# Optimization experiments

Measured on AMD Instinct MI355X. Metric: run time of the kernel, lower is better.

## Reference

```python
import jax, jax.numpy as jnp
import numpy as np
import math

MAX_SIZE = 2048  # max_size init arg


def setup_inputs() -> dict:
    key = jax.random.key(0)
    k1, k2, k3 = jax.random.split(key, 3)
    B, S, D = 16, 1024, 512
    PRED = 256
    data = jax.random.normal(k1, (B, S, D), dtype=jnp.float32)
    W = jax.random.normal(k2, (PRED, D), dtype=jnp.float32) * (1.0 / math.sqrt(D))
    b = jax.random.normal(k3, (PRED,), dtype=jnp.float32) * 0.01
    return {"data": data, "W": W, "b": b}


def reference(data, W, b):
    # data: [B, S, D]; self-attention with q=k=v=data
    B, S, D = data.shape
    pred_len = W.shape[0]
    scale = 1.0 / math.sqrt(D)
    scores = jnp.einsum('bsd,btd->bst', data, data) * scale          # [B,S,S]
    prob = jax.nn.softmax(scores, axis=-1)
    attn = jnp.einsum('bst,btd->bsd', prob, data)                     # [B,S,D]
    # NOTE: the original concatenates a 'mask' block (rows S..2S) onto attn,
    # but the per-timestep Linear loop only reads rows 0..S-1, so the mask
    # never affects the output (dead code). The loop collapses to one GEMM.
    lin = jnp.einsum('bsd,pd->bsp', attn, W) + b                      # [B,S,pred_len]
    out = jnp.zeros((B, MAX_SIZE, pred_len), dtype=data.dtype)
    out = out.at[:, :S, :].set(lin)
    return out
```

## Files before the change

### kernel.cpp

```cpp
#include <hip/hip_runtime.h>
#include <cstdint>
#include <cstddef>

#define B_    16
#define S_    1024
#define D_    512
#define P_    256
#define MAXS_ 2048

typedef unsigned short u16;
typedef unsigned int   u32;
typedef _Float16 f16;
typedef _Float16 f16x8 __attribute__((ext_vector_type(8)));
typedef float  f32x4  __attribute__((ext_vector_type(4)));
typedef unsigned short u16x4 __attribute__((ext_vector_type(4)));
typedef unsigned short u16x8 __attribute__((ext_vector_type(8)));

__device__ __forceinline__ void gld_lds16(const void* g, void* l) {
  __builtin_amdgcn_global_load_lds(
      (const __attribute__((address_space(1))) u32*)g,
      (__attribute__((address_space(3))) u32*)l, 16, 0, 0);
}

__device__ __forceinline__ u16 f2h(float f) {
  return __builtin_bit_cast(u16, (f16)f);
}
__device__ __forceinline__ float h2f(u16 h) {
  return (float)__builtin_bit_cast(f16, h);
}

template<int BPB>
__device__ __forceinline__ void xcd_map(int L, int& bz, int& r) {
  const int t = L & 7;
  const int j = L >> 3;
  bz = (t << 1) | (j / BPB);
  r  = j % BPB;
}

__global__ void convert_f16_kernel(const float* __restrict__ src, u16* __restrict__ dst, long n4) {
  long stride = (long)gridDim.x * blockDim.x;
  for (long i = (long)blockIdx.x * blockDim.x + threadIdx.x; i < n4; i += stride) {
    float4 v = ((const float4*)src)[i];
    u16x4 o;
    o[0] = f2h(v.x); o[1] = f2h(v.y); o[2] = f2h(v.z); o[3] = f2h(v.w);
    ((u16x4*)dst)[i] = o;
  }
}

__global__ __launch_bounds__(512, 2) void qk_pipe(
    const u16* __restrict__ A, u16* __restrict__ Cout,
    float2* __restrict__ rowpart, float scale) {
  extern __shared__ __align__(16) char smem[];
  const int tid  = threadIdx.x;
  const int lane = tid & 63;
  const int w    = tid >> 6;
  const int wm   = w >> 2;
  const int wn   = w & 3;
  const int lr   = lane & 15;
  const int hi   = lane >> 4;

  const int L = blockIdx.x + (blockIdx.y << 2) + (blockIdx.z << 4);
  int bz, r;
  xcd_map<16>(L, bz, r);
  const int I0 = (r >> 2) * 256;
  const int J0 = (r & 3) * 256;
  const u16* Ab = A + (long)bz * (S_ * D_);

  auto stageP = [&](int s, int part) {
    if (s >= 16) return;
    char* dst = smem + (s & 3) * 32768 + part * 16384;
    const int base = part ? J0 : I0;
    const int k0 = s * 32;
    #pragma unroll
    for (int i = 0; i < 2; ++i) {
      int cid   = i * 512 + tid;
      int inner = cid >> 2;
      int c     = (cid & 3) ^ ((inner >> 1) & 3);
      gld_lds16(Ab + (size_t)(base + inner) * D_ + k0 + c * 8, dst + cid * 16);
    }
  };

  f32x4 acc[8][4] = {};

  stageP(0, 0); stageP(0, 1);
  stageP(1, 0); stageP(1, 1);
  stageP(2, 0); stageP(2, 1);
  asm volatile("s_waitcnt vmcnt(8)" ::: "memory");
  __builtin_amdgcn_s_barrier();

  for (int s = 0; s < 16; ++s) {
    const char* sl = smem + (s & 3) * 32768;
    f16x8 af0[4], af1[4], bf[4];
    #pragma unroll
    for (int mq = 0; mq < 4; ++mq) {
      int row = wm * 128 + mq * 16 + lr;
      int cp  = hi ^ ((row >> 1) & 3);
      af0[mq] = *(const f16x8*)(sl + row * 64 + cp * 16);
    }
    #pragma unroll
    for (int mq = 0; mq < 4; ++mq) {
      int row = wm * 128 + 64 + mq * 16 + lr;
      int cp  = hi ^ ((row >> 1) & 3);
      af1[mq] = *(const f16x8*)(sl + row * 64 + cp * 16);
    }
    #pragma unroll
    for (int n = 0; n < 4; ++n) {
      int row = wn * 64 + n * 16 + lr;
      int cp  = hi ^ ((row >> 1) & 3);
      bf[n] = *(const f16x8*)(sl + 16384 + row * 64 + cp * 16);
    }
    stageP(s + 3, 0);
    stageP(s + 3, 1);
    asm volatile("s_waitcnt lgkmcnt(0)" ::: "memory");
    __builtin_amdgcn_sched_barrier(0);
    __builtin_amdgcn_s_setprio(1);
    #pragma unroll
    for (int mq = 0; mq < 4; ++mq)
      #pragma unroll
      for (int n = 0; n < 4; ++n)
        acc[mq][n] = __builtin_amdgcn_mfma_f32_16x16x32_f16(af0[mq], bf[n], acc[mq][n], 0, 0, 0);
    #pragma unroll
    for (int mq = 0; mq < 4; ++mq)
      #pragma unroll
      for (int n = 0; n < 4; ++n)
        acc[4 + mq][n] = __builtin_amdgcn_mfma_f32_16x16x32_f16(af1[mq], bf[n], acc[4 + mq][n], 0, 0, 0);
    __builtin_amdgcn_s_setprio(0);
    if (s <= 12)      asm volatile("s_waitcnt vmcnt(8)" ::: "memory");
    else if (s == 13) asm volatile("s_waitcnt vmcnt(4)" ::: "memory");
    else if (s == 14) asm volatile("s_waitcnt vmcnt(0)" ::: "memory");
    __builtin_amdgcn_s_barrier();
  }

  __syncthreads();
  float2* part = (float2*)smem;
  const float l2e = 1.4426950408889634f;
  u16* Cb = Cout + (long)bz * S_ * S_;
  const int row0 = I0 + wm * 128;
  const int col0 = J0 + wn * 64;
  #pragma unroll
  for (int m = 0; m < 8; ++m) {
    #pragma unroll
    for (int i = 0; i < 4; ++i) {
      int rr = row0 + m * 16 + (hi << 2) + i;
      float v[4];
      #pragma unroll
      for (int n = 0; n < 4; ++n) v[n] = acc[m][n][i] * scale;
      float mx = fmaxf(fmaxf(v[0], v[1]), fmaxf(v[2], v[3]));
      #pragma unroll
      for (int off = 1; off <= 8; off <<= 1)
        mx = fmaxf(mx, __shfl_xor(mx, off));
      float sum = 0.f;
      #pragma unroll
      for (int n = 0; n < 4; ++n) sum += exp2f((v[n] - mx) * l2e);
      #pragma unroll
      for (int off = 1; off <= 8; off <<= 1)
        sum += __shfl_xor(sum, off);
      #pragma unroll
      for (int n = 0; n < 4; ++n)
        Cb[(size_t)rr * S_ + col0 + n * 16 + lr] = f2h(v[n]);
      if (lr == 0)
        part[(wm * 128 + m * 16 + (hi << 2) + i) * 4 + wn] = make_float2(mx, sum);
    }
  }
  __syncthreads();
  if (tid < 256) {
    float2 a = part[tid * 4],     b = part[tid * 4 + 1];
    float2 c = part[tid * 4 + 2], d = part[tid * 4 + 3];
    float m = fmaxf(fmaxf(a.x, b.x), fmaxf(c.x, d.x));
    float l = a.y * exp2f((a.x - m) * l2e) + b.y * exp2f((b.x - m) * l2e)
            + c.y * exp2f((c.x - m) * l2e) + d.y * exp2f((d.x - m) * l2e);
    rowpart[((long)bz * 4 + (J0 >> 8)) * S_ + I0 + tid] = make_float2(m, l);
  }
}

__global__ __launch_bounds__(256, 2) void pv_slot(
    const u16* __restrict__ scores, const u16* __restrict__ VWT,
    const float2* __restrict__ rowpart,
    float* __restrict__ out, const float* __restrict__ bias) {
  extern __shared__ __align__(16) char smem[];
  const int tid  = threadIdx.x;
  const int lane = tid & 63;
  const int w    = tid >> 6;
  const int wm   = w >> 1;
  const int wn   = w & 1;
  const int lr   = lane & 15;
  const int hi   = lane >> 4;

  const int L = blockIdx.x + (blockIdx.y << 1) + (blockIdx.z << 6);
  int bz, rblk;
  xcd_map<64>(L, bz, rblk);
  const int yt = rblk >> 1;
  const int J0 = (rblk & 1) * 128;

  float* ob = out + (long)bz * MAXS_ * P_;
  if (yt >= 16) {
    #pragma unroll 2
    for (int i = tid; i < 64 * 32; i += 256) {
      int rr = i >> 5;
      int c4 = i & 31;
      *((float4*)(ob + (size_t)(yt * 64 + rr) * P_ + J0) + c4) =
          make_float4(0.f, 0.f, 0.f, 0.f);
    }
    return;
  }

  const int q0 = yt * 64;
  const u16* sA = scores + ((long)bz * S_ + q0) * S_;
  const u16* Vb = VWT + (long)bz * P_ * S_ + (size_t)J0 * S_;
  const float l2e = 1.4426950408889634f;

  const int ar0 = tid >> 3;
  const int ar1 = 32 + (tid >> 3);
  const int ac  = tid & 7;
  const int c0  = ac ^ (ar0 & 7);
  const int c1  = ac ^ (ar1 & 7);

  const float2* rp = rowpart + (long)bz * 4 * S_;
  auto mergeStat = [&](int row, float& nml, float& il) {
    float2 a = rp[row],          b = rp[S_ + row];
    float2 c = rp[2 * S_ + row], d = rp[3 * S_ + row];
    float m = fmaxf(fmaxf(a.x, b.x), fmaxf(c.x, d.x));
    float l = a.y * exp2f((a.x - m) * l2e) + b.y * exp2f((b.x - m) * l2e)
            + c.y * exp2f((c.x - m) * l2e) + d.y * exp2f((d.x - m) * l2e);
    nml = -m * l2e;
    il  = 1.f / l;
  };
  float nml0, il0, nml1, il1;
  mergeStat(q0 + ar0, nml0, il0);
  mergeStat(q0 + ar1, nml1, il1);

  auto loadA = [&](int s, u16x8 (&r)[2]) {
    r[0] = *(const u16x8*)(sA + (size_t)ar0 * S_ + s * 64 + c0 * 8);
    r[1] = *(const u16x8*)(sA + (size_t)ar1 * S_ + s * 64 + c1 * 8);
  };
  auto writeA = [&](int buf, u16x8 (&r)[2]) {
    char* dA = smem + buf * 8192;
    u16x8 p0, p1;
    #pragma unroll
    for (int j = 0; j < 8; ++j) {
      p0[j] = f2h(exp2f(fmaf(h2f(r[0][j]), l2e, nml0)) * il0);
      p1[j] = f2h(exp2f(fmaf(h2f(r[1][j]), l2e, nml1)) * il1);
    }
    *(u16x8*)(dA + (size_t)tid * 16)         = p0;
    *(u16x8*)(dA + (size_t)(256 + tid) * 16) = p1;
  };
  auto stageB = [&](int s, int buf) {
    char* dB = smem + 24576 + buf * 16384;
    #pragma unroll
    for (int i = 0; i < 4; ++i) {
      int cid = i * 256 + tid;
      int row = cid >> 3;
      int c   = (cid & 7) ^ (row & 7);
      gld_lds16(Vb + (size_t)row * S_ + s * 64 + c * 8, dB + cid * 16);
    }
  };

  f32x4 acc[2][4] = {};
  u16x8 rA[2][2];

  loadA(0, rA[0]);
  __builtin_amdgcn_sched_barrier(0);
  stageB(0, 0);
  __builtin_amdgcn_sched_barrier(0);
  loadA(1, rA[1]);
  __builtin_amdgcn_sched_barrier(0);
  stageB(1, 1);
  __builtin_amdgcn_sched_barrier(0);
  asm volatile("s_waitcnt vmcnt(6)" ::: "memory");
  writeA(0, rA[0]);
  asm volatile("s_waitcnt lgkmcnt(0)" ::: "memory");
  __builtin_amdgcn_s_barrier();

  #pragma unroll
  for (int s = 0; s < 16; ++s) {
    const int bufR = s % 3;
    const char* aB = smem + bufR * 8192;
    const char* bB = smem + 24576 + bufR * 16384;

    f16x8 af[2][2], bf[2][4];
    #pragma unroll
    for (int kk = 0; kk < 2; ++kk) {
      #pragma unroll
      for (int m = 0; m < 2; ++m) {
        int row = wm * 32 + m * 16 + lr;
        int cp  = (kk * 4 + hi) ^ (row & 7);
        af[kk][m] = *(const f16x8*)(aB + row * 128 + cp * 16);
      }
      #pragma unroll
      for (int n = 0; n < 4; ++n) {
        int row = wn * 64 + n * 16 + lr;
        int cp  = (kk * 4 + hi) ^ (row & 7);
        bf[kk][n] = *(const f16x8*)(bB + row * 128 + cp * 16);
      }
    }

    if (s + 2 < 16) {
      loadA(s + 2, rA[s & 1]);
      __builtin_amdgcn_sched_barrier(0);
      stageB(s + 2, (s + 2) % 3);
      __builtin_amdgcn_sched_barrier(0);
    }

    __builtin_amdgcn_s_setprio(1);
    #pragma unroll
    for (int kk = 0; kk < 2; ++kk)
      #pragma unroll
      for (int m = 0; m < 2; ++m)
        #pragma unroll
        for (int n = 0; n < 4; ++n)
          acc[m][n] = __builtin_amdgcn_mfma_f32_16x16x32_f16(
              af[kk][m], bf[kk][n], acc[m][n], 0, 0, 0);
    __builtin_amdgcn_s_setprio(0);

    if (s < 15) {
      if (s <= 13) asm volatile("s_waitcnt vmcnt(6)" ::: "memory");
      else         asm volatile("s_waitcnt vmcnt(0)" ::: "memory");
      writeA((s + 1) % 3, rA[(s + 1) & 1]);
      asm volatile("s_waitcnt lgkmcnt(0)" ::: "memory");
      __builtin_amdgcn_s_barrier();
    }
  }

  float bv[4];
  #pragma unroll
  for (int n = 0; n < 4; ++n) bv[n] = bias[J0 + wn * 64 + n * 16 + lr];
  #pragma unroll
  for (int m = 0; m < 2; ++m) {
    #pragma unroll
    for (int i = 0; i < 4; ++i) {
      int rr = q0 + wm * 32 + m * 16 + (hi << 2) + i;
      #pragma unroll
      for (int n = 0; n < 4; ++n)
        ob[(size_t)rr * P_ + J0 + wn * 64 + n * 16 + lr] = acc[m][n][i] + bv[n];
    }
  }
}

template<int KK, int BM, int BN, int NW, int WNS, int BPB>
__global__ __launch_bounds__(NW * 64, 2) void gemm_nt_small(
    const u16* __restrict__ A, const u16* __restrict__ Bm,
    u16* __restrict__ C, long sAb, long sBb, long sCb, int LDC) {
  constexpr int T   = NW * 64;
  constexpr int WMS = NW / WNS;
  constexpr int MF  = BM / (WMS * 16);
  constexpr int NF  = BN / (WNS * 16);
  constexpr int LA  = BM * 8 / T;
  constexpr int LB  = BN * 8 / T;
  constexpr int SZ  = (BM + BN) * 128;
  constexpr int NT  = KK / 64;

  extern __shared__ __align__(16) char smem[];
  const int tid  = threadIdx.x;
  const int lane = tid & 63;
  const int w    = tid >> 6;
  const int wm   = w / WNS;
  const int wn   = w % WNS;
  const int lr   = lane & 15;
  const int hi   = lane >> 4;

  const int L = blockIdx.x + gridDim.x * (blockIdx.y + gridDim.y * blockIdx.z);
  int bz, r;
  xcd_map<BPB>(L, bz, r);
  const int I0 = (r / gridDim.x) * BM;
  const int J0 = (r % gridDim.x) * BN;
  const u16* Ab = A  + (long)bz * sAb;
  const u16* Bb = Bm + (long)bz * sBb;

  auto stage = [&](int buf, int k0) {
    char* sA = smem + buf * SZ;
    char* sB = sA + BM * 128;
    #pragma unroll
    for (int i = 0; i < LA; ++i) {
      int cid = i * T + tid;
      int row = cid >> 3;
      int c   = (cid & 7) ^ (row & 7);
      gld_lds16(Ab + (size_t)(I0 + row) * KK + k0 + c * 8, sA + cid * 16);
    }
    #pragma unroll
    for (int i = 0; i < LB; ++i) {
      int cid = i * T + tid;
      int row = cid >> 3;
      int c   = (cid & 7) ^ (row & 7);
      gld_lds16(Bb + (size_t)(J0 + row) * KK + k0 + c * 8, sB + cid * 16);
    }
  };

  f32x4 acc[MF][NF] = {};
  stage(0, 0);
  for (int t = 0; t < NT; ++t) {
    const char* lA = smem + (t & 1) * SZ;
    const char* lB = lA + BM * 128;
    if (t + 1 < NT) {
      stage((t + 1) & 1, (t + 1) * 64);
      asm volatile("s_waitcnt vmcnt(%0)" :: "i"(LA + LB) : "memory");
    } else {
      asm volatile("s_waitcnt vmcnt(0)" ::: "memory");
    }
    __builtin_amdgcn_s_barrier();
    __builtin_amdgcn_sched_barrier(0);
    #pragma unroll
    for (int kk = 0; kk < 2; ++kk) {
      f16x8 af[MF], bfv[NF];
      #pragma unroll
      for (int m = 0; m < MF; ++m) {
        int row = wm * (MF * 16) + m * 16 + lr;
        int cp  = (kk * 4 + hi) ^ (row & 7);
        af[m] = *(const f16x8*)(lA + ((row * 8 + cp) << 4));
      }
      #pragma unroll
      for (int n = 0; n < NF; ++n) {
        int row = wn * (NF * 16) + n * 16 + lr;
        int cp  = (kk * 4 + hi) ^ (row & 7);
        bfv[n] = *(const f16x8*)(lB + ((row * 8 + cp) << 4));
      }
      __builtin_amdgcn_s_setprio(1);
      #pragma unroll
      for (int m = 0; m < MF; ++m)
        #pragma unroll
        for (int n = 0; n < NF; ++n)
          acc[m][n] = __builtin_amdgcn_mfma_f32_16x16x32_f16(af[m], bfv[n], acc[m][n], 0, 0, 0);
      __builtin_amdgcn_s_setprio(0);
    }
    __builtin_amdgcn_sched_barrier(0);
    __builtin_amdgcn_s_barrier();
  }

  const int row0 = I0 + wm * (MF * 16);
  const int col0 = J0 + wn * (NF * 16);
  #pragma unroll
  for (int m = 0; m < MF; ++m)
    #pragma unroll
    for (int i = 0; i < 4; ++i) {
      int rr = row0 + m * 16 + (hi << 2) + i;
      #pragma unroll
      for (int n = 0; n < NF; ++n)
        C[(long)bz * sCb + (size_t)rr * LDC + col0 + n * 16 + lr] = f2h(acc[m][n][i]);
    }
}

extern "C" void kernel_launch(void* const* d_in, const int* in_sizes, int n_in,
                              void* d_out, int out_size, void* d_ws, size_t ws_size,
                              hipStream_t stream) {
  const float* data = (const float*)d_in[0];
  const float* W    = (const float*)d_in[1];
  const float* bias = (const float*)d_in[2];
  float* out = (float*)d_out;
  char*  ws  = (char*)d_ws;

  const size_t MB = 1024 * 1024;
  u16*    dataH   = (u16*)(ws);
  u16*    Wh      = (u16*)(ws + 16 * MB);
  u16*    scoresH = (u16*)(ws + 17 * MB);
  u16*    VWT     = (u16*)(ws + 49 * MB);
  float2* rowpart = (float2*)(ws + 57 * MB);

  const float scale = 0.04419417382415922f;

  constexpr int SMEM_QK = 4 * 32768;
  constexpr int SMEM_PV = 3 * 8192 + 3 * 16384;
  constexpr int SMEM_VW = 2 * (64 + 128) * 128;

  (void)hipFuncSetAttribute((const void*)&qk_pipe,
                      hipFuncAttributeMaxDynamicSharedMemorySize, SMEM_QK);
  (void)hipFuncSetAttribute((const void*)&pv_slot,
                      hipFuncAttributeMaxDynamicSharedMemorySize, SMEM_PV);
  (void)hipFuncSetAttribute((const void*)&gemm_nt_small<512, 64, 128, 4, 2, 32>,
                      hipFuncAttributeMaxDynamicSharedMemorySize, SMEM_VW);

  convert_f16_kernel<<<2048, 256, 0, stream>>>(data, dataH, (long)B_ * S_ * D_ / 4);
  convert_f16_kernel<<<64, 256, 0, stream>>>(W, Wh, (long)P_ * D_ / 4);

  gemm_nt_small<512, 64, 128, 4, 2, 32><<<dim3(8, 4, 16), 256, SMEM_VW, stream>>>(
      Wh, dataH, VWT, 0L, (long)S_ * D_, (long)P_ * S_, S_);

  qk_pipe<<<dim3(4, 4, 16), 512, SMEM_QK, stream>>>(
      dataH, scoresH, rowpart, scale);

  pv_slot<<<dim3(2, 32, 16), 256, SMEM_PV, stream>>>(
      scoresH, VWT, rowpart, out, bias);
}
```

Before: 78.39 us.

## Shrink QK tile to 128x128 with 4 waves and 3-stage pipeline

The QK^T kernel moves from 256x256 tiles with 8 waves and a 4-deep LDS ring to 128x128 tiles with 4 waves and a 3-deep ring. This quadruples the grid to 1024 blocks for better CU fill and occupancy. The per-row softmax partials are now split into 8 column slices, so the PV kernel merges 8 partial max/sum pairs per row instead of 4. The smaller tiles lower arithmetic intensity and raise global and L2 traffic for the QK operands.

After: 80.42 us. +2.6%, slower.

```diff
diff --git a/kernel.cpp b/kernel.cpp
--- a/kernel.cpp
+++ b/kernel.cpp
@@ -47,86 +47,77 @@
   }
 }
 
-__global__ __launch_bounds__(512, 2) void qk_pipe(
+__global__ __launch_bounds__(256, 3) void qk_pipe(
     const u16* __restrict__ A, u16* __restrict__ Cout,
     float2* __restrict__ rowpart, float scale) {
   extern __shared__ __align__(16) char smem[];
   const int tid  = threadIdx.x;
   const int lane = tid & 63;
   const int w    = tid >> 6;
-  const int wm   = w >> 2;
-  const int wn   = w & 3;
+  const int wm   = w >> 1;
+  const int wn   = w & 1;
   const int lr   = lane & 15;
   const int hi   = lane >> 4;
 
-  const int L = blockIdx.x + (blockIdx.y << 2) + (blockIdx.z << 4);
+  const int L = blockIdx.x + (blockIdx.y << 3) + (blockIdx.z << 6);
   int bz, r;
-  xcd_map<16>(L, bz, r);
-  const int I0 = (r >> 2) * 256;
-  const int J0 = (r & 3) * 256;
+  xcd_map<64>(L, bz, r);
+  const int I0 = (r >> 3) * 128;
+  const int J0 = (r & 7) * 128;
   const u16* Ab = A + (long)bz * (S_ * D_);
 
-  auto stageP = [&](int s, int part) {
+  auto stage = [&](int s) {
     if (s >= 16) return;
-    char* dst = smem + (s & 3) * 32768 + part * 16384;
-    const int base = part ? J0 : I0;
+    char* dst = smem + (s % 3) * 16384;
     const int k0 = s * 32;
     #pragma unroll
     for (int i = 0; i < 2; ++i) {
-      int cid   = i * 512 + tid;
-      int inner = cid >> 2;
-      int c     = (cid & 3) ^ ((inner >> 1) & 3);
-      gld_lds16(Ab + (size_t)(base + inner) * D_ + k0 + c * 8, dst + cid * 16);
-    }
-  };
-
-  f32x4 acc[8][4] = {};
-
-  stageP(0, 0); stageP(0, 1);
-  stageP(1, 0); stageP(1, 1);
-  stageP(2, 0); stageP(2, 1);
-  asm volatile("s_waitcnt vmcnt(8)" ::: "memory");
+      int cid = i * 256 + tid;
+      int row = cid >> 2;
+      int c   = (cid & 3) ^ ((row >> 1) & 3);
+      gld_lds16(Ab + (size_t)(I0 + row) * D_ + k0 + c * 8, dst + cid * 16);
+    }
+    #pragma unroll
+    for (int i = 0; i < 2; ++i) {
+      int cid = i * 256 + tid;
+      int row = cid >> 2;
+      int c   = (cid & 3) ^ ((row >> 1) & 3);
+      gld_lds16(Ab + (size_t)(J0 + row) * D_ + k0 + c * 8, dst + 8192 + cid * 16);
+    }
+  };
+
+  f32x4 acc[4][4] = {};
+
+  stage(0); stage(1);
+  asm volatile("s_waitcnt vmcnt(4)" ::: "memory");
   __builtin_amdgcn_s_barrier();
 
   for (int s = 0; s < 16; ++s) {
-    const char* sl = smem + (s & 3) * 32768;
-    f16x8 af0[4], af1[4], bf[4];
-    #pragma unroll
-    for (int mq = 0; mq < 4; ++mq) {
-      int row = wm * 128 + mq * 16 + lr;
+    const char* sl = smem + (s % 3) * 16384;
+    f16x8 af[4], bf[4];
+    #pragma unroll
+    for (int m = 0; m < 4; ++m) {
+      int row = wm * 64 + m * 16 + lr;
       int cp  = hi ^ ((row >> 1) & 3);
-      af0[mq] = *(const f16x8*)(sl + row * 64 + cp * 16);
-    }
-    #pragma unroll
-    for (int mq = 0; mq < 4; ++mq) {
-      int row = wm * 128 + 64 + mq * 16 + lr;
-      int cp  = hi ^ ((row >> 1) & 3);
-      af1[mq] = *(const f16x8*)(sl + row * 64 + cp * 16);
+      af[m] = *(const f16x8*)(sl + row * 64 + cp * 16);
     }
     #pragma unroll
     for (int n = 0; n < 4; ++n) {
       int row = wn * 64 + n * 16 + lr;
       int cp  = hi ^ ((row >> 1) & 3);
-      bf[n] = *(const f16x8*)(sl + 16384 + row * 64 + cp * 16);
-    }
-    stageP(s + 3, 0);
-    stageP(s + 3, 1);
+      bf[n] = *(const f16x8*)(sl + 8192 + row * 64 + cp * 16);
+    }
+    stage(s + 2);
     asm volatile("s_waitcnt lgkmcnt(0)" ::: "memory");
     __builtin_amdgcn_sched_barrier(0);
     __builtin_amdgcn_s_setprio(1);
     #pragma unroll
-    for (int mq = 0; mq < 4; ++mq)
+    for (int m = 0; m < 4; ++m)
       #pragma unroll
       for (int n = 0; n < 4; ++n)
-        acc[mq][n] = __builtin_amdgcn_mfma_f32_16x16x32_f16(af0[mq], bf[n], acc[mq][n], 0, 0, 0);
-    #pragma unroll
-    for (int mq = 0; mq < 4; ++mq)
-      #pragma unroll
-      for (int n = 0; n < 4; ++n)
-        acc[4 + mq][n] = __builtin_amdgcn_mfma_f32_16x16x32_f16(af1[mq], bf[n], acc[4 + mq][n], 0, 0, 0);
+        acc[m][n] = __builtin_amdgcn_mfma_f32_16x16x32_f16(af[m], bf[n], acc[m][n], 0, 0, 0);
     __builtin_amdgcn_s_setprio(0);
-    if (s <= 12)      asm volatile("s_waitcnt vmcnt(8)" ::: "memory");
-    else if (s == 13) asm volatile("s_waitcnt vmcnt(4)" ::: "memory");
+    if (s <= 13)      asm volatile("s_waitcnt vmcnt(4)" ::: "memory");
     else if (s == 14) asm volatile("s_waitcnt vmcnt(0)" ::: "memory");
     __builtin_amdgcn_s_barrier();
   }
@@ -135,13 +126,14 @@
   float2* part = (float2*)smem;
   const float l2e = 1.4426950408889634f;
   u16* Cb = Cout + (long)bz * S_ * S_;
-  const int row0 = I0 + wm * 128;
+  const int row0 = I0 + wm * 64;
   const int col0 = J0 + wn * 64;
   #pragma unroll
-  for (int m = 0; m < 8; ++m) {
+  for (int m = 0; m < 4; ++m) {
     #pragma unroll
     for (int i = 0; i < 4; ++i) {
-      int rr = row0 + m * 16 + (hi << 2) + i;
+      int rl = wm * 64 + m * 16 + (hi << 2) + i;
+      int rr = I0 + rl;
       float v[4];
       #pragma unroll
       for (int n = 0; n < 4; ++n) v[n] = acc[m][n][i] * scale;
@@ -158,19 +150,17 @@
       #pragma unroll
       for (int n = 0; n < 4; ++n)
         Cb[(size_t)rr * S_ + col0 + n * 16 + lr] = f2h(v[n]);
-      if (lr == 0)
-        part[(wm * 128 + m * 16 + (hi << 2) + i) * 4 + wn] = make_float2(mx, sum);
+      if (lr == 0) part[rl * 2 + wn] = make_float2(mx, sum);
     }
   }
   __syncthreads();
-  if (tid < 256) {
-    float2 a = part[tid * 4],     b = part[tid * 4 + 1];
-    float2 c = part[tid * 4 + 2], d = part[tid * 4 + 3];
-    float m = fmaxf(fmaxf(a.x, b.x), fmaxf(c.x, d.x));
-    float l = a.y * exp2f((a.x - m) * l2e) + b.y * exp2f((b.x - m) * l2e)
-            + c.y * exp2f((c.x - m) * l2e) + d.y * exp2f((d.x - m) * l2e);
-    rowpart[((long)bz * 4 + (J0 >> 8)) * S_ + I0 + tid] = make_float2(m, l);
-  }
+  if (tid < 128) {
+    float2 a = part[tid * 2], b = part[tid * 2 + 1];
+    float m = fmaxf(a.x, b.x);
+    float l = a.y * exp2f((a.x - m) * l2e) + b.y * exp2f((b.x - m) * l2e);
+    rowpart[((long)bz * 8 + (J0 >> 7)) * S_ + I0 + tid] = make_float2(m, l);
+  }
+  (void)row0;
 }
 
 __global__ __launch_bounds__(256, 2) void pv_slot(
@@ -215,13 +205,19 @@
   const int c0  = ac ^ (ar0 & 7);
   const int c1  = ac ^ (ar1 & 7);
 
-  const float2* rp = rowpart + (long)bz * 4 * S_;
+  const float2* rp = rowpart + (long)bz * 8 * S_;
   auto mergeStat = [&](int row, float& nml, float& il) {
-    float2 a = rp[row],          b = rp[S_ + row];
-    float2 c = rp[2 * S_ + row], d = rp[3 * S_ + row];
-    float m = fmaxf(fmaxf(a.x, b.x), fmaxf(c.x, d.x));
-    float l = a.y * exp2f((a.x - m) * l2e) + b.y * exp2f((b.x - m) * l2e)
-            + c.y * exp2f((c.x - m) * l2e) + d.y * exp2f((d.x - m) * l2e);
+    float2 p[8];
+    float m = -3.4e38f;
+    #pragma unroll
+    for (int jx = 0; jx < 8; ++jx) {
+      p[jx] = rp[jx * S_ + row];
+      m = fmaxf(m, p[jx].x);
+    }
+    float l = 0.f;
+    #pragma unroll
+    for (int jx = 0; jx < 8; ++jx)
+      l += p[jx].y * exp2f((p[jx].x - m) * l2e);
     nml = -m * l2e;
     il  = 1.f / l;
   };
@@ -456,7 +452,7 @@
 
   const float scale = 0.04419417382415922f;
 
-  constexpr int SMEM_QK = 4 * 32768;
+  constexpr int SMEM_QK = 3 * 16384;
   constexpr int SMEM_PV = 3 * 8192 + 3 * 16384;
   constexpr int SMEM_VW = 2 * (64 + 128) * 128;
 
@@ -473,7 +469,7 @@
   gemm_nt_small<512, 64, 128, 4, 2, 32><<<dim3(8, 4, 16), 256, SMEM_VW, stream>>>(
       Wh, dataH, VWT, 0L, (long)S_ * D_, (long)P_ * S_, S_);
 
-  qk_pipe<<<dim3(4, 4, 16), 512, SMEM_QK, stream>>>(
+  qk_pipe<<<dim3(8, 8, 16), 256, SMEM_QK, stream>>>(
       dataH, scoresH, rowpart, scale);
 
   pv_slot<<<dim3(2, 32, 16), 256, SMEM_PV, stream>>>(
```
